# Optimization experiments

Measured on AMD Instinct MI355X. Metric: run time of the kernel, lower is better.

The kernel has to match this reference:

```python
import jax, jax.numpy as jnp
import numpy as np
import math

B, S, D = 4, 2048, 1024
H, DK = 16, 64
NUM_BUCKETS = 32
MAX_DISTANCE = 128


def _relative_position_bucket(relative_position, num_buckets=NUM_BUCKETS, max_distance=MAX_DISTANCE):
    # Bidirectional (encoder) variant, matching TFT5Attention._relative_position_bucket
    nb = num_buckets // 2
    rel_buckets = (relative_position > 0).astype(jnp.int32) * nb
    rel = jnp.abs(relative_position)
    max_exact = nb // 2
    is_small = rel < max_exact
    rel_if_large = max_exact + (
        jnp.log(jnp.maximum(rel, 1).astype(jnp.float32) / max_exact)
        / math.log(max_distance / max_exact)
        * (nb - max_exact)
    ).astype(jnp.int32)
    rel_if_large = jnp.minimum(rel_if_large, nb - 1)
    return rel_buckets + jnp.where(is_small, rel, rel_if_large)


def compute_bias(rel_bias, q_len, k_len):
    context = jnp.arange(q_len)[:, None]
    memory = jnp.arange(k_len)[None, :]
    buckets = _relative_position_bucket(memory - context)  # [q_len, k_len]
    values = rel_bias[buckets]                              # [q_len, k_len, H]
    return jnp.transpose(values, (2, 0, 1))[None]           # [1, H, q_len, k_len]


def setup_inputs() -> dict:
    key = jax.random.key(0)
    ks = jax.random.split(key, 6)
    scale = 1.0 / math.sqrt(D)
    return {
        "hidden_states": jax.random.normal(ks[0], (B, S, D), dtype=jnp.float32),
        "Wq": jax.random.normal(ks[1], (D, H * DK), dtype=jnp.float32) * scale,
        "Wk": jax.random.normal(ks[2], (D, H * DK), dtype=jnp.float32) * scale,
        "Wv": jax.random.normal(ks[3], (D, H * DK), dtype=jnp.float32) * scale,
        "Wo": jax.random.normal(ks[4], (H * DK, D), dtype=jnp.float32) * scale,
        "rel_bias": jax.random.normal(ks[5], (NUM_BUCKETS, H), dtype=jnp.float32),
    }


def reference(hidden_states, Wq, Wk, Wv, Wo, rel_bias):
    b, s, _ = hidden_states.shape

    def to_heads(x):  # [b, s, H*DK] -> [b, H, s, DK]
        return jnp.transpose(x.reshape(b, s, H, DK), (0, 2, 1, 3))

    q = to_heads(hidden_states @ Wq)
    k = to_heads(hidden_states @ Wk)
    v = to_heads(hidden_states @ Wv)

    # NOTE: T5 does NOT scale scores by 1/sqrt(d_kv)
    scores = jnp.einsum("bhqd,bhkd->bhqk", q, k)
    scores = scores + compute_bias(rel_bias, s, s)
    weights = jax.nn.softmax(scores, axis=-1)
    attn = jnp.einsum("bhqk,bhkd->bhqd", weights, v)
    attn = jnp.transpose(attn, (0, 2, 1, 3)).reshape(b, s, H * DK)
    return attn @ Wo
```

## Files before the change

kernel.cpp:

```cpp
#include <hip/hip_runtime.h>
#include <hip/hip_bf16.h>
#include <cstdint>

#define DI __device__ __forceinline__

typedef __attribute__((ext_vector_type(4))) float f32x4;
typedef __attribute__((ext_vector_type(16))) float f32x16;
typedef __attribute__((ext_vector_type(8))) short s16x8;
typedef __attribute__((ext_vector_type(4))) short s16x4;
typedef __attribute__((ext_vector_type(4))) unsigned int u32x4;
typedef unsigned int u32;

constexpr int Sc = 2048;
constexpr float LOG2E = 1.44269504088896340736f;

DI short f2bf(float x) {
    __hip_bfloat16 h = __float2bfloat16(x);
    return __builtin_bit_cast(short, h);
}
DI float bf2f(short x) {
    __hip_bfloat16 h = __builtin_bit_cast(__hip_bfloat16, x);
    return __bfloat162float(h);
}
DI u32 pack2(float a, float b) {
    return (u32)(unsigned short)f2bf(a) | ((u32)(unsigned short)f2bf(b) << 16);
}
DI void pl32swap(u32& a, u32& b) {
    asm("v_permlane32_swap_b32 %0, %1" : "+v"(a), "+v"(b));
}

DI void cp16(const short* g, short* l) {
    __builtin_amdgcn_global_load_lds(
        (const __attribute__((address_space(1))) u32*)g,
        (__attribute__((address_space(3))) u32*)l, 16, 0, 0);
}

DI float fexp2(float x) {
#if __has_builtin(__builtin_amdgcn_exp2f)
    return __builtin_amdgcn_exp2f(x);
#else
    return exp2f(x);
#endif
}
DI float frcp(float x) {
#if __has_builtin(__builtin_amdgcn_rcpf)
    return __builtin_amdgcn_rcpf(x);
#else
    return 1.0f / x;
#endif
}

__global__ void xconv_kernel(const float* __restrict__ X, short* __restrict__ X2) {
    size_t i = ((size_t)blockIdx.x * 256 + threadIdx.x) * 4;
    float4 v = *reinterpret_cast<const float4*>(X + i);
    int m = (int)(i >> 10);
    int k = (int)(i & 1023);
    float vv[4] = {v.x, v.y, v.z, v.w};
    short hi[4], lo[4];
#pragma unroll
    for (int j = 0; j < 4; ++j) { hi[j] = f2bf(vv[j]); lo[j] = f2bf(vv[j] - bf2f(hi[j])); }
    s16x4 h4 = {hi[0], hi[1], hi[2], hi[3]};
    s16x4 l4 = {lo[0], lo[1], lo[2], lo[3]};
    *reinterpret_cast<s16x4*>(X2 + (size_t)m * 2048 + k) = h4;
    *reinterpret_cast<s16x4*>(X2 + (size_t)m * 2048 + 1024 + k) = l4;
}

__global__ void wqkv_conv(const float* __restrict__ Wq, const float* __restrict__ Wk,
                          const float* __restrict__ Wv, short* __restrict__ WT2) {
    __shared__ float t[32][33];
    int z = blockIdx.z;
    const float* W = (z == 0) ? Wq : (z == 1 ? Wk : Wv);
    int k0 = blockIdx.x * 32, n0 = blockIdx.y * 32;
    int tx = threadIdx.x, ty = threadIdx.y;
#pragma unroll
    for (int i = 0; i < 4; ++i)
        t[ty + 8 * i][tx] = W[(size_t)(k0 + ty + 8 * i) * 1024 + n0 + tx];
    __syncthreads();
#pragma unroll
    for (int i = 0; i < 4; ++i) {
        float v = t[tx][ty + 8 * i];
        short hi = f2bf(v), lo = f2bf(v - bf2f(hi));
        size_t r = (size_t)(z * 1024 + n0 + ty + 8 * i) * 2048 + k0 + tx;
        WT2[r] = hi;
        WT2[r + 1024] = lo;
    }
}

__global__ void wo_conv(const float* __restrict__ Wo, short* __restrict__ WoT) {
    __shared__ float t[32][33];
    int k0 = blockIdx.x * 32, n0 = blockIdx.y * 32;
    int tx = threadIdx.x, ty = threadIdx.y;
#pragma unroll
    for (int i = 0; i < 4; ++i)
        t[ty + 8 * i][tx] = Wo[(size_t)(k0 + ty + 8 * i) * 1024 + n0 + tx];
    __syncthreads();
#pragma unroll
    for (int i = 0; i < 4; ++i)
        WoT[(size_t)(n0 + ty + 8 * i) * 1024 + k0 + tx] = f2bf(t[tx][ty + 8 * i]);
}

__global__ void bias_kernel(const float* __restrict__ rel_bias, short* __restrict__ tab) {
    int idx = blockIdx.x * 256 + threadIdx.x;
    int h = idx >> 12;
    int i = idx & 4095;
    int delta = i - 2047;
    int ad = delta < 0 ? -delta : delta;
    int b;
    if (ad < 8) b = ad;
    else if (ad < 12) b = 8;
    else if (ad < 16) b = 9;
    else if (ad < 23) b = 10;
    else if (ad < 32) b = 11;
    else if (ad < 46) b = 12;
    else if (ad < 64) b = 13;
    else if (ad < 91) b = 14;
    else b = 15;
    if (delta > 0) b += 16;
    tab[idx] = f2bf(rel_bias[b * 16 + h] * LOG2E);
}

template <int EPI>
__launch_bounds__(256)
__global__ void gemm_bt(const short* __restrict__ A, const short* __restrict__ Bt,
                        int K, int lda, int ldb, int aWrap, int bWrap,
                        float* __restrict__ C, int ldc,
                        short* __restrict__ q2, short* __restrict__ k2, short* __restrict__ vt) {
    __shared__ __align__(16) short As[128 * 32];
    __shared__ __align__(16) short Bs[128 * 32];
    const int tid = threadIdx.x;
    const int w = tid >> 6, l = tid & 63;
    const int m0 = blockIdx.x * 128, n0 = blockIdx.y * 128;
    const int wm = (w >> 1) * 64, wn = (w & 1) * 64;
    const int ar = tid >> 2, ac = (tid & 3) * 8;
    const int wb = w * 512;

    const int region = (EPI == 1) ? (n0 >> 10) : 0;

    f32x4 acc[4][4];
#pragma unroll
    for (int i = 0; i < 4; ++i)
#pragma unroll
        for (int j = 0; j < 4; ++j) acc[i][j] = (f32x4){0.f, 0.f, 0.f, 0.f};

    const int nk = K / 32;
    const int nkUse = (EPI == 1) ? (region == 2 ? 32 : 64) : nk;
    for (int kt = 0; kt < nkUse; ++kt) {
        int kk = kt * 32;
        int ca = kk - (kk >= aWrap ? aWrap : 0);
        int cb = kk - (kk >= bWrap ? bWrap : 0);
        cp16(A + (size_t)(m0 + ar) * lda + ca + ac, As + wb);
        cp16(A + (size_t)(m0 + 64 + ar) * lda + ca + ac, As + 2048 + wb);
        cp16(Bt + (size_t)(n0 + ar) * ldb + cb + ac, Bs + wb);
        cp16(Bt + (size_t)(n0 + 64 + ar) * ldb + cb + ac, Bs + 2048 + wb);
        __syncthreads();
        s16x8 af[4], bfv[4];
#pragma unroll
        for (int i = 0; i < 4; ++i)
            af[i] = *reinterpret_cast<const s16x8*>(As + (wm + i * 16 + (l & 15)) * 32 + (l >> 4) * 8);
#pragma unroll
        for (int i = 0; i < 4; ++i)
            bfv[i] = *reinterpret_cast<const s16x8*>(Bs + (wn + i * 16 + (l & 15)) * 32 + (l >> 4) * 8);
#pragma unroll
        for (int mi = 0; mi < 4; ++mi)
#pragma unroll
            for (int ni = 0; ni < 4; ++ni)
                acc[mi][ni] = __builtin_amdgcn_mfma_f32_16x16x32_bf16(af[mi], bfv[ni], acc[mi][ni], 0, 0, 0);
        __syncthreads();
    }

    const int rl = l >> 4, cl = l & 15;
    if (EPI == 0) {
#pragma unroll
        for (int mi = 0; mi < 4; ++mi) {
            int row = m0 + wm + mi * 16 + rl * 4;
#pragma unroll
            for (int ni = 0; ni < 4; ++ni) {
                int col = n0 + wn + ni * 16 + cl;
#pragma unroll
                for (int r = 0; r < 4; ++r)
                    C[(size_t)(row + r) * ldc + col] = acc[mi][ni][r];
            }
        }
    } else {
#pragma unroll
        for (int mi = 0; mi < 4; ++mi) {
#pragma unroll
            for (int ni = 0; ni < 4; ++ni) {
#pragma unroll
                for (int r = 0; r < 4; ++r) {
                    int m = m0 + wm + mi * 16 + rl * 4 + r;
                    int n = (n0 & 1023) + wn + ni * 16 + cl;
                    int bb = m >> 11, s = m & 2047;
                    int h = n >> 6, d = n & 63;
                    int bh = bb * 16 + h;
                    float c = acc[mi][ni][r];
                    if (region == 0) {
                        c *= LOG2E;
                        short hi = f2bf(c);
                        short lo = f2bf(c - bf2f(hi));
                        size_t base = ((size_t)bh * 2048 + s) * 128;
                        q2[base + d] = hi;
                        q2[base + 64 + d] = lo;
                    } else if (region == 1) {
                        k2[((size_t)bh * 2048 + s) * 64 + d] = f2bf(c);
                    } else {
                        vt[((size_t)bh * 64 + d) * 2048 + s] = f2bf(c);
                    }
                }
            }
        }
    }
}

__launch_bounds__(512, 4)
__global__ void flash_kernel(const short* __restrict__ q2, const short* __restrict__ k2,
                             const short* __restrict__ vt, const short* __restrict__ btab,
                             short* __restrict__ attnb) {
    __shared__ __align__(16) short Ks[2][4096];
    __shared__ __align__(16) short Vs[2][4096];
    __shared__ __align__(16) short Bsh0[2304];
    __shared__ __align__(16) short Bsh1[2304];

    const int tid = threadIdx.x;
    const int w = tid >> 6, l = tid & 63;
    const int l31 = l & 31, hi = l >> 5;

    const int L = blockIdx.x;
    const int xcd = L & 7, idx = L >> 3;
    const int bh = xcd + 8 * (idx & 7);
    const int qb = idx >> 3;
    const int h = bh & 15;
    const int q0b = qb * 256;
    const int qw0 = q0b + w * 32;
    const int qL = w * 32 + l31;

    const short* Q = q2 + (size_t)bh * Sc * 128;
    const short* Kp = k2 + (size_t)bh * Sc * 64;
    const short* V = vt + (size_t)bh * 64 * Sc;

    {
        int base = h * 4096 + 1792 - q0b;
        for (int i = tid; i < 2304; i += 512) Bsh0[i] = btab[base + i];
        for (int i = tid; i < 2302; i += 512) Bsh1[i] = btab[base + i + 1];
    }

    auto stage = [&](int buf, int it2) {
        int kv0 = it2 * 64;
        {
            int o = w * 64 + l;
            int r = o >> 3, cs = o & 7;
            int cg = cs ^ (r & 7);
            cp16(Kp + (size_t)(kv0 + r) * 64 + cg * 8, &Ks[buf][(w * 64) * 8]);
        }
        {
            int o = w * 64 + l;
            int d = o >> 3, cs = o & 7;
            int cg = cs ^ (d & 7);
            cp16(V + (size_t)d * 2048 + kv0 + cg * 8, &Vs[buf][(w * 64) * 8]);
        }
    };

    s16x8 qf[8];
#pragma unroll
    for (int c = 0; c < 8; ++c)
        qf[c] = *reinterpret_cast<const s16x8*>(Q + (size_t)(qw0 + l31) * 128 + c * 16 + hi * 8);

    f32x16 accO[2];
#pragma unroll
    for (int i = 0; i < 16; ++i) { accO[0][i] = 0.f; accO[1][i] = 0.f; }
    float psum = 0.f;

    stage(0, 0);
    __syncthreads();

    for (int it = 0; it < 32; ++it) {
        const int cur = it & 1;
        if (it + 1 < 32) stage(cur ^ 1, it + 1);
        const int kv0 = it * 64;
#pragma unroll
        for (int T = 0; T < 2; ++T) {
            const int rA = T * 32 + l31;
            const int rsw = rA & 7;
            const short* kbase = &Ks[cur][rA * 64];
            s16x8 kh[4];
#pragma unroll
            for (int c = 0; c < 4; ++c)
                kh[c] = *reinterpret_cast<const s16x8*>(kbase + ((c * 2 + hi) ^ rsw) * 8);
            f32x16 acc = {0.f,0.f,0.f,0.f,0.f,0.f,0.f,0.f,0.f,0.f,0.f,0.f,0.f,0.f,0.f,0.f};
#pragma unroll
            for (int c = 0; c < 4; ++c)
                acc = __builtin_amdgcn_mfma_f32_32x32x16_bf16(kh[c], qf[c], acc, 0, 0, 0);
#pragma unroll
            for (int c = 0; c < 4; ++c)
                acc = __builtin_amdgcn_mfma_f32_32x32x16_bf16(kh[c], qf[c + 4], acc, 0, 0, 0);
#pragma unroll
            for (int t2 = 0; t2 < 2; ++t2) {
                u32 pk[4];
#pragma unroll
                for (int i = 0; i < 4; ++i) {
                    const int ii = t2 * 4 + i;
                    const int pstart = ((ii & 1) * 2) + ((ii >> 1) * 8);
                    const int kvg = kv0 + T * 32 + pstart + 4 * hi;
                    const int i0 = kvg - qL + 255;
                    const short* bp = (i0 & 1) ? (Bsh1 + (i0 - 1)) : (Bsh0 + i0);
                    const u32 pr2 = *reinterpret_cast<const u32*>(bp);
                    const float b0 = bf2f((short)(pr2 & 0xffff));
                    const float b1 = bf2f((short)(pr2 >> 16));
                    const int r0 = t2 * 8 + i * 2;
                    const float e0 = fexp2(acc[r0] + b0);
                    const float e1 = fexp2(acc[r0 + 1] + b1);
                    psum += e0 + e1;
                    pk[i] = pack2(e0, e1);
                }
                pl32swap(pk[0], pk[2]);
                pl32swap(pk[1], pk[3]);
                u32x4 pv4 = {pk[0], pk[1], pk[2], pk[3]};
                s16x8 pfrag = __builtin_bit_cast(s16x8, pv4);
                const int tg = T * 2 + t2;
#pragma unroll
                for (int dt = 0; dt < 2; ++dt) {
                    const int d = dt * 32 + l31;
                    s16x8 vf = *reinterpret_cast<const s16x8*>(
                        &Vs[cur][d * 64 + ((tg * 2 + hi) ^ (d & 7)) * 8]);
                    accO[dt] = __builtin_amdgcn_mfma_f32_32x32x16_bf16(pfrag, vf, accO[dt], 0, 0, 0);
                }
            }
        }
        __syncthreads();
    }

    psum += __shfl_xor(psum, 32);

    const int bb = bh >> 4;
#pragma unroll
    for (int r = 0; r < 16; ++r) {
        const int qloc = (r & 3) + 8 * (r >> 2) + 4 * hi;
        const float inv = frcp(__shfl(psum, qloc));
        const size_t rowbase = ((size_t)(bb * 2048 + qw0 + qloc)) * 1024 + h * 64;
#pragma unroll
        for (int dt = 0; dt < 2; ++dt)
            attnb[rowbase + dt * 32 + l31] = f2bf(accO[dt][r] * inv);
    }
}

extern "C" void kernel_launch(void* const* d_in, const int* in_sizes, int n_in,
                              void* d_out, int out_size, void* d_ws, size_t ws_size,
                              hipStream_t stream) {
    const float* X = (const float*)d_in[0];
    const float* Wq = (const float*)d_in[1];
    const float* Wk = (const float*)d_in[2];
    const float* Wv = (const float*)d_in[3];
    const float* Wo = (const float*)d_in[4];
    const float* RB = (const float*)d_in[5];

    char* ws = (char*)d_ws;
    size_t off = 0;
    auto alloc = [&](size_t bytes) {
        void* p = ws + off;
        off += (bytes + 255) & ~(size_t)255;
        return p;
    };
    short* X2 = (short*)alloc((size_t)8192 * 2048 * 2);
    short* WT2 = (short*)alloc((size_t)3072 * 2048 * 2);
    short* q2 = (short*)alloc((size_t)64 * 2048 * 128 * 2);
    short* k2 = (short*)alloc((size_t)64 * 2048 * 64 * 2);
    short* vt = (short*)alloc((size_t)64 * 64 * 2048 * 2);
    short* attn = (short*)alloc((size_t)8192 * 1024 * 2);
    short* WoT = (short*)alloc((size_t)1024 * 1024 * 2);
    short* btab = (short*)alloc((size_t)16 * 4096 * 2);

    xconv_kernel<<<8192, 256, 0, stream>>>(X, X2);
    wqkv_conv<<<dim3(32, 32, 3), dim3(32, 8), 0, stream>>>(Wq, Wk, Wv, WT2);
    wo_conv<<<dim3(32, 32), dim3(32, 8), 0, stream>>>(Wo, WoT);
    bias_kernel<<<256, 256, 0, stream>>>(RB, btab);
    gemm_bt<1><<<dim3(64, 24), 256, 0, stream>>>(X2, WT2, 3072, 2048, 2048, 1024, 2048,
                                                 nullptr, 0, q2, k2, vt);
    flash_kernel<<<512, 512, 0, stream>>>(q2, k2, vt, btab, attn);
    gemm_bt<0><<<dim3(64, 8), 256, 0, stream>>>(attn, WoT, 1024, 1024, 1024, 1 << 30, 1 << 30,
                                                (float*)d_out, 1024, nullptr, nullptr, nullptr);
}
```

Measured before the change: 304.4 us.

## Drop X low-part split and deepen GEMM K-tile with swizzled LDS

The input conversion now writes only the bf16 high part of X, halving the X2 buffer and its lda, so the QKV projection no longer reads a low-part correction term for X. The GEMM K-tile grows from 32 to 64, with an XOR-swizzled shared-memory layout meant to avoid bank conflicts, and each barrier pair now covers two MFMA k-steps. This cuts global traffic and synchronisation per FLOP, but dropping the X low part lowers the accuracy of the Q/K/V projections, which may affect tolerance.

Result: faster. 290.8 us (-4.5%).

```diff
diff --git a/kernel.cpp b/kernel.cpp
--- a/kernel.cpp
+++ b/kernel.cpp
@@ -53,16 +53,8 @@
 __global__ void xconv_kernel(const float* __restrict__ X, short* __restrict__ X2) {
     size_t i = ((size_t)blockIdx.x * 256 + threadIdx.x) * 4;
     float4 v = *reinterpret_cast<const float4*>(X + i);
-    int m = (int)(i >> 10);
-    int k = (int)(i & 1023);
-    float vv[4] = {v.x, v.y, v.z, v.w};
-    short hi[4], lo[4];
-#pragma unroll
-    for (int j = 0; j < 4; ++j) { hi[j] = f2bf(vv[j]); lo[j] = f2bf(vv[j] - bf2f(hi[j])); }
-    s16x4 h4 = {hi[0], hi[1], hi[2], hi[3]};
-    s16x4 l4 = {lo[0], lo[1], lo[2], lo[3]};
-    *reinterpret_cast<s16x4*>(X2 + (size_t)m * 2048 + k) = h4;
-    *reinterpret_cast<s16x4*>(X2 + (size_t)m * 2048 + 1024 + k) = l4;
+    s16x4 h4 = {f2bf(v.x), f2bf(v.y), f2bf(v.z), f2bf(v.w)};
+    *reinterpret_cast<s16x4*>(X2 + i) = h4;
 }
 
 __global__ void wqkv_conv(const float* __restrict__ Wq, const float* __restrict__ Wk,
@@ -125,14 +117,13 @@
                         int K, int lda, int ldb, int aWrap, int bWrap,
                         float* __restrict__ C, int ldc,
                         short* __restrict__ q2, short* __restrict__ k2, short* __restrict__ vt) {
-    __shared__ __align__(16) short As[128 * 32];
-    __shared__ __align__(16) short Bs[128 * 32];
+    __shared__ __align__(16) short As[128 * 64];
+    __shared__ __align__(16) short Bs[128 * 64];
     const int tid = threadIdx.x;
     const int w = tid >> 6, l = tid & 63;
     const int m0 = blockIdx.x * 128, n0 = blockIdx.y * 128;
     const int wm = (w >> 1) * 64, wn = (w & 1) * 64;
-    const int ar = tid >> 2, ac = (tid & 3) * 8;
-    const int wb = w * 512;
+    const int rl = l >> 4, cl = l & 15;
 
     const int region = (EPI == 1) ? (n0 >> 10) : 0;
 
@@ -142,33 +133,45 @@
 #pragma unroll
         for (int j = 0; j < 4; ++j) acc[i][j] = (f32x4){0.f, 0.f, 0.f, 0.f};
 
-    const int nk = K / 32;
-    const int nkUse = (EPI == 1) ? (region == 2 ? 32 : 64) : nk;
+    const int nk = K / 64;
+    const int nkUse = (EPI == 1) ? (region == 2 ? 16 : 32) : nk;
+
+    const int o0 = w * 64 + l;
+    const int sr0 = o0 >> 3;
+    const int scg = (o0 & 7) ^ (sr0 & 7);
+
+    const int sw = cl & 7;
+
     for (int kt = 0; kt < nkUse; ++kt) {
-        int kk = kt * 32;
+        int kk = kt * 64;
         int ca = kk - (kk >= aWrap ? aWrap : 0);
         int cb = kk - (kk >= bWrap ? bWrap : 0);
-        cp16(A + (size_t)(m0 + ar) * lda + ca + ac, As + wb);
-        cp16(A + (size_t)(m0 + 64 + ar) * lda + ca + ac, As + 2048 + wb);
-        cp16(Bt + (size_t)(n0 + ar) * ldb + cb + ac, Bs + wb);
-        cp16(Bt + (size_t)(n0 + 64 + ar) * ldb + cb + ac, Bs + 2048 + wb);
+#pragma unroll
+        for (int j = 0; j < 4; ++j) {
+            int r = j * 32 + sr0;
+            cp16(A + (size_t)(m0 + r) * lda + ca + scg * 8, As + (j * 256 + w * 64) * 8);
+            cp16(Bt + (size_t)(n0 + r) * ldb + cb + scg * 8, Bs + (j * 256 + w * 64) * 8);
+        }
         __syncthreads();
-        s16x8 af[4], bfv[4];
-#pragma unroll
-        for (int i = 0; i < 4; ++i)
-            af[i] = *reinterpret_cast<const s16x8*>(As + (wm + i * 16 + (l & 15)) * 32 + (l >> 4) * 8);
-#pragma unroll
-        for (int i = 0; i < 4; ++i)
-            bfv[i] = *reinterpret_cast<const s16x8*>(Bs + (wn + i * 16 + (l & 15)) * 32 + (l >> 4) * 8);
-#pragma unroll
-        for (int mi = 0; mi < 4; ++mi)
-#pragma unroll
-            for (int ni = 0; ni < 4; ++ni)
-                acc[mi][ni] = __builtin_amdgcn_mfma_f32_16x16x32_bf16(af[mi], bfv[ni], acc[mi][ni], 0, 0, 0);
+#pragma unroll
+        for (int ks = 0; ks < 2; ++ks) {
+            const int slot = ((ks << 2) | rl) ^ sw;
+            s16x8 af[4], bfv[4];
+#pragma unroll
+            for (int i = 0; i < 4; ++i)
+                af[i] = *reinterpret_cast<const s16x8*>(As + (wm + i * 16 + cl) * 64 + slot * 8);
+#pragma unroll
+            for (int i = 0; i < 4; ++i)
+                bfv[i] = *reinterpret_cast<const s16x8*>(Bs + (wn + i * 16 + cl) * 64 + slot * 8);
+#pragma unroll
+            for (int mi = 0; mi < 4; ++mi)
+#pragma unroll
+                for (int ni = 0; ni < 4; ++ni)
+                    acc[mi][ni] = __builtin_amdgcn_mfma_f32_16x16x32_bf16(af[mi], bfv[ni], acc[mi][ni], 0, 0, 0);
+        }
         __syncthreads();
     }
 
-    const int rl = l >> 4, cl = l & 15;
     if (EPI == 0) {
 #pragma unroll
         for (int mi = 0; mi < 4; ++mi) {
@@ -360,7 +363,7 @@
         off += (bytes + 255) & ~(size_t)255;
         return p;
     };
-    short* X2 = (short*)alloc((size_t)8192 * 2048 * 2);
+    short* X2 = (short*)alloc((size_t)8192 * 1024 * 2);
     short* WT2 = (short*)alloc((size_t)3072 * 2048 * 2);
     short* q2 = (short*)alloc((size_t)64 * 2048 * 128 * 2);
     short* k2 = (short*)alloc((size_t)64 * 2048 * 64 * 2);
@@ -373,7 +376,7 @@
     wqkv_conv<<<dim3(32, 32, 3), dim3(32, 8), 0, stream>>>(Wq, Wk, Wv, WT2);
     wo_conv<<<dim3(32, 32), dim3(32, 8), 0, stream>>>(Wo, WoT);
     bias_kernel<<<256, 256, 0, stream>>>(RB, btab);
-    gemm_bt<1><<<dim3(64, 24), 256, 0, stream>>>(X2, WT2, 3072, 2048, 2048, 1024, 2048,
+    gemm_bt<1><<<dim3(64, 24), 256, 0, stream>>>(X2, WT2, 3072, 1024, 2048, 1024, 2048,
                                                  nullptr, 0, q2, k2, vt);
     flash_kernel<<<512, 512, 0, stream>>>(q2, k2, vt, btab, attn);
     gemm_bt<0><<<dim3(64, 8), 256, 0, stream>>>(attn, WoT, 1024, 1024, 1024, 1 << 30, 1 << 30,
```
